# Optimization experiments

Measured on AMD Instinct MI355X. Metric: run time of the kernel, lower is better.

## Reference

```python
import jax, jax.numpy as jnp
import numpy as np

T, WS, SHIFT, HEADS, DIM = 5, (8, 8), (4, 4), 6, 192
HEAD_DIM = DIM // HEADS
SCALE = HEAD_DIM ** -0.5
MLP_HID = 4 * DIM
TABLE_LEN = (T * 2 * WS[0] - 1) * (2 * WS[1] - 1)


def _rel_index():
    # exact replica of WindowAttention.__init__ index construction (t,h,w coords)
    ct, ch, cw = np.arange(T), np.arange(WS[0]), np.arange(WS[1])
    coords = np.stack(np.meshgrid(ct, ch, cw, indexing='ij')).reshape(3, -1)
    rel = (coords[:, :, None] - coords[:, None, :]).transpose(1, 2, 0).astype(np.int64)
    rel[:, :, 0] += WS[0] - 1
    rel[:, :, 1] += WS[1] - 1
    rel[:, :, 0] *= 2 * WS[1] - 1
    return jnp.asarray(rel.sum(-1))  # (N, N)


def _attn_mask(H, W):
    # standard shifted-window mask on (H,W); identical across T, so tile (T,T)
    img = np.zeros((H, W), np.float32)
    cnt = 0
    for hs in (slice(0, -WS[0]), slice(-WS[0], -SHIFT[0]), slice(-SHIFT[0], None)):
        for ws_ in (slice(0, -WS[1]), slice(-WS[1], -SHIFT[1]), slice(-SHIFT[1], None)):
            img[hs, ws_] = cnt
            cnt += 1
    img = img.reshape(H // WS[0], WS[0], W // WS[1], WS[1]).transpose(0, 2, 1, 3)
    img = img.reshape(-1, WS[0] * WS[1])  # (nW, Wh*Ww)
    m = img[:, None, :] - img[:, :, None]
    m = np.where(m != 0, -100.0, 0.0).astype(np.float32)
    return jnp.asarray(np.tile(m, (1, T, T)))  # (nW, T*Wh*Ww, T*Wh*Ww)


def _win_part(x, ws):
    B, t, H, W, C = x.shape
    x = x.reshape(B, t, H // ws[0], ws[0], W // ws[1], ws[1], C)
    return x.transpose(0, 2, 4, 1, 3, 5, 6).reshape(-1, t * ws[0] * ws[1], C)


def _win_rev(w, ws, H, W, t, B):
    x = w.reshape(B, H // ws[0], W // ws[1], t, ws[0], ws[1], -1)
    return x.transpose(0, 3, 1, 4, 2, 5, 6).reshape(B, t, H, W, -1)


def _ln(x, g, b):
    mu = x.mean(-1, keepdims=True)
    var = ((x - mu) ** 2).mean(-1, keepdims=True)
    return (x - mu) * jax.lax.rsqrt(var + 1e-5) * g + b


def _forward(x, ln1_g, ln1_b, qkv_w, qkv_b, rel_bias_table, proj_w, proj_b,
             ln2_g, ln2_b, fc1_w, fc1_b, fc2_w, fc2_b, H, W):
    B, L, C = x.shape
    shortcut = x
    h = _ln(x, ln1_g, ln1_b)
    qkv = h @ qkv_w.T + qkv_b                                   # (B, L, 3C)
    qkv = qkv.reshape(B, T, H, W, 3 * C)
    qkv = jnp.roll(qkv, (-SHIFT[0], -SHIFT[1]), axis=(2, 3))
    qkv = _win_part(qkv, WS)                                    # (B_, N, 3C)
    B_, N, _ = qkv.shape
    qkv = qkv.reshape(B_, N, 3, HEADS, HEAD_DIM).transpose(2, 0, 3, 1, 4)
    q, k, v = qkv[0], qkv[1], qkv[2]
    attn = jnp.einsum('bhnd,bhmd->bhnm', q * SCALE, k)          # (B_, H, N, N)
    bias = rel_bias_table[_rel_index()].transpose(2, 0, 1)      # (heads, N, N)
    attn = attn + bias[None]
    mask = _attn_mask(H, W)                                     # (nW, N, N)
    nW = mask.shape[0]
    attn = attn.reshape(B_ // nW, nW, HEADS, N, N) + mask[None, :, None]
    attn = jax.nn.softmax(attn.reshape(B_, HEADS, N, N), axis=-1)
    out = jnp.einsum('bhnm,bhmd->bhnd', attn, v)
    out = out.transpose(0, 2, 1, 3).reshape(B_, N, C)
    out = out @ proj_w.T + proj_b
    out = _win_rev(out, WS, H, W, T, B)
    out = jnp.roll(out, (SHIFT[0], SHIFT[1]), axis=(2, 3)).reshape(B, L, C)
    x = shortcut + out
    h = _ln(x, ln2_g, ln2_b)
    h = jax.nn.gelu(h @ fc1_w.T + fc1_b, approximate=False) @ fc2_w.T + fc2_b
    return x + h


def setup_inputs() -> dict:
    key = jax.random.key(0)
    ks = jax.random.split(key, 8)
    B, Himg, Wimg = 2, 64, 64
    L = T * Himg * Wimg
    s = 0.02
    return {
        'x': jax.random.normal(ks[0], (B, L, DIM), jnp.float32),
        'ln1_g': jnp.ones((DIM,), jnp.float32),
        'ln1_b': jnp.zeros((DIM,), jnp.float32),
        'qkv_w': jax.random.normal(ks[1], (3 * DIM, DIM), jnp.float32) * s,
        'qkv_b': jnp.zeros((3 * DIM,), jnp.float32),
        'rel_bias_table': jax.random.normal(ks[2], (TABLE_LEN, HEADS), jnp.float32) * s,
        'proj_w': jax.random.normal(ks[3], (DIM, DIM), jnp.float32) * s,
        'proj_b': jnp.zeros((DIM,), jnp.float32),
        'ln2_g': jnp.ones((DIM,), jnp.float32),
        'ln2_b': jnp.zeros((DIM,), jnp.float32),
        'fc1_w': jax.random.normal(ks[4], (MLP_HID, DIM), jnp.float32) * s,
        'fc1_b': jnp.zeros((MLP_HID,), jnp.float32),
        'fc2_w': jax.random.normal(ks[5], (DIM, MLP_HID), jnp.float32) * s,
        'fc2_b': jnp.zeros((DIM,), jnp.float32),
        'H': Himg,
        'W': Wimg,
    }


def reference(x, ln1_g, ln1_b, qkv_w, qkv_b, rel_bias_table, proj_w, proj_b,
              ln2_g, ln2_b, fc1_w, fc1_b, fc2_w, fc2_b, H, W):
    return _forward(x, ln1_g, ln1_b, qkv_w, qkv_b, rel_bias_table, proj_w, proj_b,
                    ln2_g, ln2_b, fc1_w, fc1_b, fc2_w, fc2_b, H, W)
```

## Files before the change

### kernel.cpp

```cpp
#include <hip/hip_runtime.h>
#include <math.h>

typedef unsigned short u16;
typedef unsigned int u32;
typedef short bf16x8 __attribute__((ext_vector_type(8)));
typedef float f32x4 __attribute__((ext_vector_type(4)));
typedef _Float16 f16x4 __attribute__((ext_vector_type(4)));

#define TT 5
#define HEADS 6
#define HD 32
#define DIM 192
#define NWIN 320
#define LTOK (TT*64*64)
#define BATCH 2
#define MROWS (BATCH*LTOK)
#define QSCALE 0.17677669529663687f
#define LOG2E 1.4426950408889634f
#define QSCALE2 (QSCALE * LOG2E)
#define MASK2 (-100.0f * LOG2E)

__device__ __forceinline__ u16 f2bf(float f) {
    u32 u = __float_as_uint(f);
    u32 r = (u + 0x7FFFu + ((u >> 16) & 1u)) >> 16;
    return (u16)r;
}
__device__ __forceinline__ float bflo(u32 u) { return __uint_as_float(u << 16); }
__device__ __forceinline__ float bfhi(u32 u) { return __uint_as_float(u & 0xFFFF0000u); }
__device__ __forceinline__ u32 pkh(float a, float b) {
    auto h = __builtin_amdgcn_cvt_pkrtz(a, b);
    return __builtin_bit_cast(u32, h);
}
#if __has_builtin(__builtin_amdgcn_exp2f)
__device__ __forceinline__ float ex2(float x) { return __builtin_amdgcn_exp2f(x); }
#else
__device__ __forceinline__ float ex2(float x) {
    float r; asm("v_exp_f32 %0, %1" : "=v"(r) : "v"(x)); return r;
}
#endif

__global__ __launch_bounds__(256) void cvt4_kernel(
    const float* __restrict__ a, const float* __restrict__ b,
    const float* __restrict__ c, const float* __restrict__ d,
    u16* __restrict__ oa, u16* __restrict__ ob,
    u16* __restrict__ oc, u16* __restrict__ od)
{
    int i = blockIdx.x * 256 + threadIdx.x;
    if (i < 110592)       oa[i]          = f2bf(a[i]);
    else if (i < 147456)  ob[i - 110592] = f2bf(b[i - 110592]);
    else if (i < 294912)  oc[i - 147456] = f2bf(c[i - 147456]);
    else                  od[i - 294912] = f2bf(d[i - 294912]);
}

__global__ __launch_bounds__(256) void ln_kernel(
    const float* __restrict__ x, const float* __restrict__ g,
    const float* __restrict__ b, u16* __restrict__ out)
{
    int tok  = blockIdx.x * 4 + (threadIdx.x >> 6);
    int lane = threadIdx.x & 63;
    const float* xr = x + (size_t)tok * DIM;
    float v0 = xr[lane], v1 = xr[lane + 64], v2 = xr[lane + 128];
    float s = v0 + v1 + v2;
    #pragma unroll
    for (int off = 32; off; off >>= 1) s += __shfl_xor(s, off, 64);
    float mu = s * (1.0f / 192.0f);
    float d0 = v0 - mu, d1 = v1 - mu, d2 = v2 - mu;
    float vs = d0 * d0 + d1 * d1 + d2 * d2;
    #pragma unroll
    for (int off = 32; off; off >>= 1) vs += __shfl_xor(vs, off, 64);
    float rstd = rsqrtf(vs * (1.0f / 192.0f) + 1e-5f);
    u16* orow = out + (size_t)tok * DIM;
    orow[lane]       = f2bf(d0 * rstd * g[lane]       + b[lane]);
    orow[lane + 64]  = f2bf(d1 * rstd * g[lane + 64]  + b[lane + 64]);
    orow[lane + 128] = f2bf(d2 * rstd * g[lane + 128] + b[lane + 128]);
}

template<int EPI>
__global__ __launch_bounds__(256) void mfma_gemm(
    const u16* __restrict__ A, const u16* __restrict__ W,
    const float* __restrict__ bias, void* __restrict__ outp,
    const float* __restrict__ xin, int N, int K)
{
    __shared__ u16 As[128 * 64];
    __shared__ u16 Bs[64 * 64];
    const int tid  = threadIdx.x;
    const int lane = tid & 63, wv = tid >> 6;
    const int ln16 = lane & 15, quad = lane >> 4;

    const int flat  = blockIdx.y * gridDim.x + blockIdx.x;
    const int cpx   = (gridDim.x * gridDim.y) >> 3;
    const int nf    = (flat & 7) * cpx + (flat >> 3);
    const int bn    = nf % gridDim.x;
    const int bm    = nf / gridDim.x;

    const int srow = lane >> 3;
    const int sxor = (lane & 7) ^ srow;
    const int acol = sxor * 8;

    f32x4 acc[2][4] = {};

    for (int k0 = 0; k0 < K; k0 += 64) {
        __syncthreads();
        #pragma unroll
        for (int a = 0; a < 4; ++a) {
            const u16* g = A + (size_t)(bm * 128 + a * 32 + wv * 8 + srow) * K + k0 + acol;
            __builtin_amdgcn_global_load_lds(
                (const __attribute__((address_space(1))) u32*)g,
                (__attribute__((address_space(3))) u32*)((char*)As + a * 4096 + wv * 1024),
                16, 0, 0);
        }
        #pragma unroll
        for (int bb = 0; bb < 2; ++bb) {
            const u16* g = W + (size_t)(bn * 64 + bb * 32 + wv * 8 + srow) * K + k0 + acol;
            __builtin_amdgcn_global_load_lds(
                (const __attribute__((address_space(1))) u32*)g,
                (__attribute__((address_space(3))) u32*)((char*)Bs + bb * 4096 + wv * 1024),
                16, 0, 0);
        }
        __syncthreads();
        #pragma unroll
        for (int s = 0; s < 2; ++s) {
            bf16x8 af[2], bf[4];
            #pragma unroll
            for (int i = 0; i < 2; ++i) {
                int r = wv * 32 + i * 16 + ln16;
                int slot = (s * 4 + quad) ^ (r & 7);
                af[i] = *(const bf16x8*)((const char*)As + r * 128 + slot * 16);
            }
            #pragma unroll
            for (int j = 0; j < 4; ++j) {
                int r = j * 16 + ln16;
                int slot = (s * 4 + quad) ^ (r & 7);
                bf[j] = *(const bf16x8*)((const char*)Bs + r * 128 + slot * 16);
            }
            #pragma unroll
            for (int i = 0; i < 2; ++i)
                #pragma unroll
                for (int j = 0; j < 4; ++j)
                    acc[i][j] = __builtin_amdgcn_mfma_f32_16x16x32_bf16(
                        af[i], bf[j], acc[i][j], 0, 0, 0);
        }
    }

    #pragma unroll
    for (int i = 0; i < 2; ++i) {
        int gr0 = bm * 128 + wv * 32 + i * 16 + quad * 4;
        #pragma unroll
        for (int j = 0; j < 4; ++j) {
            int gc = bn * 64 + j * 16 + ln16;
            float bv = bias[gc];
            #pragma unroll
            for (int rr = 0; rr < 4; ++rr) {
                int gr = gr0 + rr;
                float val = acc[i][j][rr] + bv;
                if (EPI == 0) {
                    ((u16*)outp)[(size_t)gr * N + gc] = f2bf(val);
                } else if (EPI == 1) {
                    float gl = val * 0.5f * (1.0f + erff(val * 0.70710678118654752f));
                    ((u16*)outp)[(size_t)gr * N + gc] = f2bf(gl);
                } else if (EPI == 2) {
                    int b_ = gr / NWIN, n = gr - b_ * NWIN;
                    int b = b_ >> 6, hb = (b_ >> 3) & 7, wb = b_ & 7;
                    int t = n >> 6, hi = (n >> 3) & 7, wj = n & 7;
                    int hs = (hb * 8 + hi + 4) & 63;
                    int wsrc = (wb * 8 + wj + 4) & 63;
                    size_t dst = ((size_t)b * LTOK + t * 4096 + hs * 64 + wsrc) * DIM + gc;
                    ((float*)outp)[dst] = xin[dst] + val;
                } else {
                    ((float*)outp)[(size_t)gr * N + gc] += val;
                }
            }
        }
    }
}

__global__ __launch_bounds__(320) void attn_kernel(
    const u16* __restrict__ qkv, const float* __restrict__ table,
    u16* __restrict__ attout)
{
    const int head = blockIdx.x % HEADS;
    const int b_   = blockIdx.x / HEADS;
    const int b = b_ >> 6, hb = (b_ >> 3) & 7, wb = b_ & 7;
    const int tid = threadIdx.x;
    const int lane = tid & 63, wv = tid >> 6;
    const int ln16 = lane & 15, quad = lane >> 4;

    __shared__ u16 Ks[320 * 40];
    __shared__ u16 Vt[32 * 328];
    __shared__ u16 meta[320];
    __shared__ float tbl[188];

    {
        int n = tid;
        int t1 = n >> 6, r1 = (n >> 3) & 7, c1 = n & 7;
        int h1 = hb * 8 + r1, w1 = wb * 8 + c1;
        int l1 = t1 * 4096 + ((h1 + 4) & 63) * 64 + ((w1 + 4) & 63);
        const u16* src = qkv + ((size_t)b * LTOK + l1) * (3 * DIM) + head * HD;
        const uint4* k4 = (const uint4*)(src + DIM);
        #pragma unroll
        for (int i = 0; i < 4; ++i)
            *(uint4*)(Ks + n * 40 + i * 8) = k4[i];
        const uint4* v4 = (const uint4*)(src + 2 * DIM);
        #pragma unroll
        for (int i = 0; i < 4; ++i) {
            uint4 u = v4[i];
            u32 ws[4] = {u.x, u.y, u.z, u.w};
            #pragma unroll
            for (int j = 0; j < 4; ++j) {
                u32 hb2 = pkh(bflo(ws[j]), bfhi(ws[j]));
                int d = i * 8 + j * 2;
                Vt[d * 328 + n]       = (u16)(hb2 & 0xFFFF);
                Vt[(d + 1) * 328 + n] = (u16)(hb2 >> 16);
            }
        }
        int off = (7 - t1) * 15 + 7 - r1 - c1;
        int rh = h1 < 56 ? 0 : (h1 < 60 ? 1 : 2);
        int rw = w1 < 56 ? 0 : (w1 < 60 ? 1 : 2);
        meta[n] = (u16)(off | ((rh * 3 + rw) << 8));
        if (n < 187) tbl[n] = table[n * HEADS + head] * LOG2E;
    }

    bf16x8 qf[4];
    int basen[4], myreg[4];
    #pragma unroll
    for (int qt = 0; qt < 4; ++qt) {
        int nq = wv * 64 + qt * 16 + ln16;
        int t1 = nq >> 6, r1 = (nq >> 3) & 7, c1 = nq & 7;
        int h1 = hb * 8 + r1, w1 = wb * 8 + c1;
        int l1 = t1 * 4096 + ((h1 + 4) & 63) * 64 + ((w1 + 4) & 63);
        qf[qt] = *(const bf16x8*)(qkv + ((size_t)b * LTOK + l1) * (3 * DIM)
                                  + head * HD + quad * 8);
        basen[qt] = t1 * 15 + r1 + c1;
        int rh = h1 < 56 ? 0 : (h1 < 60 ? 1 : 2);
        int rw = w1 < 56 ? 0 : (w1 < 60 ? 1 : 2);
        myreg[qt] = rh * 3 + rw;
    }

    __syncthreads();

    f32x4 o[4][2] = {};
    float l_[4] = {};
    const f32x4 zero = {};

    #pragma unroll 1
    for (int c = 0; c < 10; ++c) {
        int kb = c * 32;
        bf16x8 af0 = *(const bf16x8*)(Ks + (kb + ln16) * 40 + quad * 8);
        bf16x8 af1 = *(const bf16x8*)(Ks + (kb + 16 + ln16) * 40 + quad * 8);
        f16x4 va[2][2];
        #pragma unroll
        for (int dt = 0; dt < 2; ++dt)
            #pragma unroll
            for (int kt = 0; kt < 2; ++kt)
                va[dt][kt] = *(const f16x4*)(Vt + (dt * 16 + ln16) * 328
                                             + kb + kt * 16 + quad * 4);
        ushort4 m4a = *(const ushort4*)(meta + kb + quad * 4);
        ushort4 m4b = *(const ushort4*)(meta + kb + 16 + quad * 4);
        u16 mta[4] = {m4a.x, m4a.y, m4a.z, m4a.w};
        u16 mtb[4] = {m4b.x, m4b.y, m4b.z, m4b.w};

        #pragma unroll
        for (int qt = 0; qt < 4; ++qt) {
            f32x4 s0 = __builtin_amdgcn_mfma_f32_16x16x32_bf16(af0, qf[qt], zero, 0, 0, 0);
            f32x4 s1 = __builtin_amdgcn_mfma_f32_16x16x32_bf16(af1, qf[qt], zero, 0, 0, 0);
            float p[8];
            #pragma unroll
            for (int r = 0; r < 4; ++r) {
                int ma = mta[r], mb = mtb[r];
                float va0 = fmaf(s0[r], QSCALE2, tbl[basen[qt] + (ma & 0xFF)]);
                float vb0 = fmaf(s1[r], QSCALE2, tbl[basen[qt] + (mb & 0xFF)]);
                p[r]     = va0 + (((ma >> 8) == myreg[qt]) ? 0.0f : MASK2);
                p[4 + r] = vb0 + (((mb >> 8) == myreg[qt]) ? 0.0f : MASK2);
            }
            float ls = 0.0f;
            #pragma unroll
            for (int j = 0; j < 8; ++j) { p[j] = ex2(p[j]); ls += p[j]; }
            l_[qt] += ls;
            uint2 pk0 = { pkh(p[0], p[1]), pkh(p[2], p[3]) };
            uint2 pk1 = { pkh(p[4], p[5]), pkh(p[6], p[7]) };
            f16x4 pf0 = __builtin_bit_cast(f16x4, pk0);
            f16x4 pf1 = __builtin_bit_cast(f16x4, pk1);
            #pragma unroll
            for (int dt = 0; dt < 2; ++dt) {
                o[qt][dt] = __builtin_amdgcn_mfma_f32_16x16x16f16(va[dt][0], pf0, o[qt][dt], 0, 0, 0);
                o[qt][dt] = __builtin_amdgcn_mfma_f32_16x16x16f16(va[dt][1], pf1, o[qt][dt], 0, 0, 0);
            }
        }
    }

    #pragma unroll
    for (int qt = 0; qt < 4; ++qt) {
        float lt = l_[qt];
        lt += __shfl_xor(lt, 16, 64);
        lt += __shfl_xor(lt, 32, 64);
        float inv = 1.0f / lt;
        int nq = wv * 64 + qt * 16 + ln16;
        u16* dst = attout + ((size_t)(b_ * NWIN + nq)) * DIM + head * HD + quad * 4;
        #pragma unroll
        for (int dt = 0; dt < 2; ++dt) {
            u32 w0 = (u32)f2bf(o[qt][dt][0] * inv) | ((u32)f2bf(o[qt][dt][1] * inv) << 16);
            u32 w1 = (u32)f2bf(o[qt][dt][2] * inv) | ((u32)f2bf(o[qt][dt][3] * inv) << 16);
            uint2 st = {w0, w1};
            *(uint2*)(dst + dt * 16) = st;
        }
    }
}

extern "C" void kernel_launch(void* const* d_in, const int* in_sizes, int n_in,
                              void* d_out, int out_size, void* d_ws, size_t ws_size,
                              hipStream_t stream)
{
    (void)in_sizes; (void)n_in; (void)out_size; (void)ws_size;
    const float* x      = (const float*)d_in[0];
    const float* ln1_g  = (const float*)d_in[1];
    const float* ln1_b  = (const float*)d_in[2];
    const float* qkv_w  = (const float*)d_in[3];
    const float* qkv_b  = (const float*)d_in[4];
    const float* table  = (const float*)d_in[5];
    const float* proj_w = (const float*)d_in[6];
    const float* proj_b = (const float*)d_in[7];
    const float* ln2_g  = (const float*)d_in[8];
    const float* ln2_b  = (const float*)d_in[9];
    const float* fc1_w  = (const float*)d_in[10];
    const float* fc1_b  = (const float*)d_in[11];
    const float* fc2_w  = (const float*)d_in[12];
    const float* fc2_b  = (const float*)d_in[13];
    float* out = (float*)d_out;

    u16* wsu     = (u16*)d_ws;
    u16* h_buf   = wsu;
    u16* qkv_buf = wsu + (size_t)MROWS * DIM;
    u16* att_buf = wsu + (size_t)MROWS * (4 * DIM);
    u16* fc1_buf = wsu + (size_t)MROWS * DIM;
    u16* wq = wsu + (size_t)MROWS * (5 * DIM);
    u16* wp = wq + 3 * DIM * DIM;
    u16* w1 = wp + DIM * DIM;
    u16* w2 = w1 + 4 * DIM * DIM;

    cvt4_kernel<<<(12 * DIM * DIM) / 256, 256, 0, stream>>>(
        qkv_w, proj_w, fc1_w, fc2_w, wq, wp, w1, w2);

    ln_kernel<<<MROWS / 4, 256, 0, stream>>>(x, ln1_g, ln1_b, h_buf);
    mfma_gemm<0><<<dim3(3 * DIM / 64, MROWS / 128), 256, 0, stream>>>(
        h_buf, wq, qkv_b, qkv_buf, nullptr, 3 * DIM, DIM);
    attn_kernel<<<128 * HEADS, 320, 0, stream>>>(qkv_buf, table, att_buf);
    mfma_gemm<2><<<dim3(DIM / 64, MROWS / 128), 256, 0, stream>>>(
        att_buf, wp, proj_b, out, x, DIM, DIM);
    ln_kernel<<<MROWS / 4, 256, 0, stream>>>(out, ln2_g, ln2_b, h_buf);
    mfma_gemm<1><<<dim3(4 * DIM / 64, MROWS / 128), 256, 0, stream>>>(
        h_buf, w1, fc1_b, fc1_buf, nullptr, 4 * DIM, DIM);
    mfma_gemm<3><<<dim3(DIM / 64, MROWS / 128), 256, 0, stream>>>(
        fc1_buf, w2, fc2_b, out, nullptr, DIM, 4 * DIM);
}
```

Measured before the change: 255.1 us.

## Double-buffer LDS tiles in MFMA GEMM to overlap global loads with compute

Splits the GEMM main loop into stage and compute steps and adds a second LDS buffer for the A and B tiles. The next K-tile is prefetched with global_load_lds while the current tile is multiplied, and a partial vmcnt wait lets the older loads finish without waiting on the new ones. The goal is to hide global memory latency behind MFMA work. LDS use doubles to 48KB per block, which may lower occupancy, and correctness depends on the vmcnt(6) count matching the six loads issued per stage.

Result: slower. 265.1 us (+3.9%).

```diff
diff --git a/kernel.cpp b/kernel.cpp
--- a/kernel.cpp
+++ b/kernel.cpp
@@ -81,8 +81,8 @@
     const float* __restrict__ bias, void* __restrict__ outp,
     const float* __restrict__ xin, int N, int K)
 {
-    __shared__ u16 As[128 * 64];
-    __shared__ u16 Bs[64 * 64];
+    __shared__ u16 As[2][128 * 64];
+    __shared__ u16 Bs[2][64 * 64];
     const int tid  = threadIdx.x;
     const int lane = tid & 63, wv = tid >> 6;
     const int ln16 = lane & 15, quad = lane >> 4;
@@ -99,14 +99,13 @@
 
     f32x4 acc[2][4] = {};
 
-    for (int k0 = 0; k0 < K; k0 += 64) {
-        __syncthreads();
+    auto stage = [&](int buf, int k0) {
         #pragma unroll
         for (int a = 0; a < 4; ++a) {
             const u16* g = A + (size_t)(bm * 128 + a * 32 + wv * 8 + srow) * K + k0 + acol;
             __builtin_amdgcn_global_load_lds(
                 (const __attribute__((address_space(1))) u32*)g,
-                (__attribute__((address_space(3))) u32*)((char*)As + a * 4096 + wv * 1024),
+                (__attribute__((address_space(3))) u32*)((char*)&As[buf][0] + a * 4096 + wv * 1024),
                 16, 0, 0);
         }
         #pragma unroll
@@ -114,10 +113,12 @@
             const u16* g = W + (size_t)(bn * 64 + bb * 32 + wv * 8 + srow) * K + k0 + acol;
             __builtin_amdgcn_global_load_lds(
                 (const __attribute__((address_space(1))) u32*)g,
-                (__attribute__((address_space(3))) u32*)((char*)Bs + bb * 4096 + wv * 1024),
+                (__attribute__((address_space(3))) u32*)((char*)&Bs[buf][0] + bb * 4096 + wv * 1024),
                 16, 0, 0);
         }
-        __syncthreads();
+    };
+
+    auto compute = [&](int c) {
         #pragma unroll
         for (int s = 0; s < 2; ++s) {
             bf16x8 af[2], bf[4];
@@ -125,13 +126,13 @@
             for (int i = 0; i < 2; ++i) {
                 int r = wv * 32 + i * 16 + ln16;
                 int slot = (s * 4 + quad) ^ (r & 7);
-                af[i] = *(const bf16x8*)((const char*)As + r * 128 + slot * 16);
+                af[i] = *(const bf16x8*)((const char*)&As[c][0] + r * 128 + slot * 16);
             }
             #pragma unroll
             for (int j = 0; j < 4; ++j) {
                 int r = j * 16 + ln16;
                 int slot = (s * 4 + quad) ^ (r & 7);
-                bf[j] = *(const bf16x8*)((const char*)Bs + r * 128 + slot * 16);
+                bf[j] = *(const bf16x8*)((const char*)&Bs[c][0] + r * 128 + slot * 16);
             }
             #pragma unroll
             for (int i = 0; i < 2; ++i)
@@ -140,7 +141,24 @@
                     acc[i][j] = __builtin_amdgcn_mfma_f32_16x16x32_bf16(
                         af[i], bf[j], acc[i][j], 0, 0, 0);
         }
-    }
+    };
+
+    const int nk = K >> 6;
+    stage(0, 0);
+    int cur = 0;
+    #pragma unroll 1
+    for (int k = 0; k < nk - 1; ++k) {
+        stage(cur ^ 1, (k + 1) << 6);
+        asm volatile("s_waitcnt vmcnt(6)" ::: "memory");
+        __builtin_amdgcn_s_barrier();
+        compute(cur);
+        asm volatile("" ::: "memory");
+        __builtin_amdgcn_s_barrier();
+        cur ^= 1;
+    }
+    asm volatile("s_waitcnt vmcnt(0)" ::: "memory");
+    __builtin_amdgcn_s_barrier();
+    compute(cur);
 
     #pragma unroll
     for (int i = 0; i < 2; ++i) {
```
